# Kernel optimization log

Measured on AMD Instinct MI355X. Metric: run time of the kernel, lower is better.

## Reference

```python
import jax, jax.numpy as jnp
import numpy as np

S, B, I = 512, 32, 512
H, O = 512, 512
TOP_K = 5
TRUNC = 100
EPS = 1e-7
NEG = -1e9


def setup_inputs() -> dict:
    key = jax.random.key(0)
    ks = jax.random.split(key, 12)
    std = 1.0 / np.sqrt(H)
    return {
        "input": jax.random.normal(ks[0], (S, B, I), jnp.float32),
        "h0": jax.random.normal(ks[1], (1, B, H), jnp.float32),
        "c0": jax.random.normal(ks[2], (1, B, H), jnp.float32),
        "mem0": jax.random.normal(ks[3], (1, B, H), jnp.float32),
        # LSTMCell params (PyTorch layout: gates ordered i, f, g, o)
        "w_ih": jax.random.uniform(ks[4], (4 * H, I), jnp.float32, -std, std),
        "w_hh": jax.random.uniform(ks[5], (4 * H, H), jnp.float32, -std, std),
        "b_ih": jax.random.uniform(ks[6], (4 * H,), jnp.float32, -std, std),
        "b_hh": jax.random.uniform(ks[7], (4 * H,), jnp.float32, -std, std),
        # attention scorer, init N(0, 0.01)
        "w_t": jax.random.normal(ks[8], (2 * H, 1), jnp.float32) * 0.01,
        "fc_w": jax.random.uniform(ks[9], (O, 2 * H), jnp.float32, -1.0 / np.sqrt(2 * H), 1.0 / np.sqrt(2 * H)),
        "fc_b": jax.random.uniform(ks[10], (O,), jnp.float32, -1.0 / np.sqrt(2 * H), 1.0 / np.sqrt(2 * H)),
    }


def _sab_forward(input, h0, c0, mem0, w_ih, w_hh, b_ih, b_hh, w_t, fc_w, fc_b):
    seq_len, batch, _ = input.shape
    hid = w_hh.shape[1]
    m0 = mem0.shape[0]
    mmax = m0 + seq_len  # remem_every_k == 1: one append per step
    mem_buf = jnp.zeros((mmax, batch, hid), input.dtype).at[:m0].set(mem0)
    pos = jnp.arange(mmax)

    def step(carry, xs):
        h, c, mem = carry
        x, i = xs
        trunc = ((i + 1) % TRUNC) == 0
        h_in = jnp.where(trunc, jax.lax.stop_gradient(h), h)
        c_in = jnp.where(trunc, jax.lax.stop_gradient(c), c)
        # LSTM cell
        gates = x @ w_ih.T + b_ih + h_in @ w_hh.T + b_hh
        gi, gf, gg, go = jnp.split(gates, 4, axis=1)
        c_new = jax.nn.sigmoid(gf) * c_in + jax.nn.sigmoid(gi) * jnp.tanh(gg)
        h_new = jax.nn.sigmoid(go) * jnp.tanh(c_new)
        # attention over current (valid) memory
        cur = m0 + i  # valid memory entries before appending
        valid = (pos < cur)[:, None]  # (mmax, 1)
        feat = jnp.tanh(jnp.concatenate([jnp.broadcast_to(h_new[None], (mmax, batch, hid)), mem], axis=2))
        scores = jnp.einsum("mbf,fo->mb", feat, w_t)  # (mmax, batch)
        s_mask = jnp.where(valid, scores, NEG)
        kth = jax.lax.top_k(s_mask.T, TOP_K)[0][:, -1]  # (batch,)
        min_valid = jnp.min(jnp.where(valid, scores, jnp.inf), axis=0)
        delta = jnp.where(cur <= TOP_K, min_valid, kth) + EPS
        aw = jnp.clip(s_mask - delta[None, :], 0.0)  # invalid rows -> 0
        aw = aw / (jnp.sum(aw, axis=0, keepdims=True) + EPS)
        m_t = jnp.einsum("mb,mbh->bh", aw, mem)
        h_out = h_new + m_t
        mem = jax.lax.dynamic_update_slice(mem, h_out[None], (cur, 0, 0))
        return (h_out, c_new, mem), (h_out, m_t)

    (h_f, c_f, mem_f), (h_seq, m_seq) = jax.lax.scan(
        step, (h0[0], c0[0], mem_buf), (input, jnp.arange(seq_len)))
    out = jnp.concatenate([h_seq, m_seq], axis=2) @ fc_w.T + fc_b  # (S,B,O)
    return out, h_f[None], c_f[None], mem_f


def reference(input, h0, c0, mem0, w_ih, w_hh, b_ih, b_hh, w_t, fc_w, fc_b):
    return _sab_forward(input, h0, c0, mem0, w_ih, w_hh, b_ih, b_hh, w_t, fc_w, fc_b)
```

## Files before the change

kernel.cpp:

```cpp
#include <hip/hip_runtime.h>

#define SEQ   512
#define NB    32
#define NH    512
#define BH    16384
#define EPSF  1e-7f
#define NWG   64

#define HF_OFF  8388608
#define CF_OFF  8404992
#define MEM_OFF 8421376

#define X0_OFF   0ul
#define X1_OFF   16777216ul
#define WI0_OFF  33554432ul
#define WI1_OFF  35651584ul
#define HH_OFF   37748736ul
#define HMF_OFF  54558720ul
#define MSEQ_OFF 71368704ul
#define FCW_OFF  88145920ul
#define S2P_OFF  89194496ul
#define BAR_OFF  93396992ul
#define GX_OFF   93405184ul

typedef __attribute__((ext_vector_type(8))) short bf16x8;
typedef __attribute__((ext_vector_type(4))) float f32x4;
typedef __attribute__((ext_vector_type(4))) int   i32x4;

__device__ __forceinline__ unsigned short f2bf(float f){
  unsigned u = __float_as_uint(f);
  unsigned r = (u + 0x7fffu + ((u >> 16) & 1u)) >> 16;
  return (unsigned short)r;
}
__device__ __forceinline__ float bf2f(unsigned short h){
  return __uint_as_float(((unsigned)h) << 16);
}
__device__ __forceinline__ float sigmf(float x){ return 1.f/(1.f + __expf(-x)); }
__device__ __forceinline__ float tanhff(float x){
  x = fminf(20.f, fmaxf(-20.f, x));
  float e = __expf(-2.f*x);
  return (1.f - e)/(1.f + e);
}

__device__ __forceinline__ void store16_cc(void* p, i32x4 v){
  asm volatile("global_store_dwordx4 %0, %1, off sc0 sc1" :: "v"(p), "v"(v) : "memory");
}

__global__ void phase0(const float* __restrict__ x, const float* __restrict__ h0,
                       const float* __restrict__ mem0, const float* __restrict__ fcw,
                       const float* __restrict__ wih,
                       unsigned short* __restrict__ x0, unsigned short* __restrict__ x1,
                       unsigned short* __restrict__ wi0, unsigned short* __restrict__ wi1,
                       unsigned short* __restrict__ hh, unsigned short* __restrict__ hmf,
                       unsigned short* __restrict__ fcwb,
                       float* __restrict__ mem_row0, unsigned* __restrict__ bar){
  long i = (long)blockIdx.x * blockDim.x + threadIdx.x;
  if (i < (long)SEQ*BH){
    float v = x[i];
    unsigned short a = f2bf(v);
    x0[i]=a; x1[i]=f2bf(v - bf2f(a));
  }
  if (i < 2048*512){
    float v = wih[i];
    unsigned short a = f2bf(v);
    wi0[i]=a; wi1[i]=f2bf(v - bf2f(a));
  }
  if (i < 512*1024) fcwb[i] = f2bf(fcw[i]);
  if (i < BH){
    float h = h0[i];
    unsigned short a = f2bf(h);
    int b = (int)(i >> 9), col = (int)(i & 511);
    long d = (long)(col>>3)*256 + b*8 + (col&7);
    hh[d]=a; hmf[d]=f2bf(h - bf2f(a));
    mem_row0[i] = mem0[i];
  }
  if (i < 2048) bar[i] = 0u;
}

__launch_bounds__(256)
__global__ void xgemm(const unsigned short* __restrict__ x0, const unsigned short* __restrict__ x1,
                      const unsigned short* __restrict__ wi0, const unsigned short* __restrict__ wi1,
                      const float* __restrict__ bih, const float* __restrict__ bhh,
                      float* __restrict__ gx){
  const int tid = threadIdx.x;
  const int wave = tid >> 6, lane = tid & 63, quad = lane >> 4, ln = lane & 15;
  const int rowb = blockIdx.x*64 + wave*16;
  const int colb = blockIdx.y*64;
  const long aoff = (long)(rowb + ln)*512 + quad*8;
  f32x4 acc[4] = {{0,0,0,0},{0,0,0,0},{0,0,0,0},{0,0,0,0}};
  #pragma unroll 4
  for (int ki = 0; ki < 16; ++ki){
    bf16x8 a0 = *(const bf16x8*)(x0 + aoff + ki*32);
    bf16x8 a1 = *(const bf16x8*)(x1 + aoff + ki*32);
    #pragma unroll
    for (int n = 0; n < 4; ++n){
      long bo = (long)(colb + n*16 + ln)*512 + quad*8 + ki*32;
      bf16x8 b0 = *(const bf16x8*)(wi0 + bo);
      bf16x8 b1 = *(const bf16x8*)(wi1 + bo);
      acc[n] = __builtin_amdgcn_mfma_f32_16x16x32_bf16(a0, b0, acc[n], 0,0,0);
      acc[n] = __builtin_amdgcn_mfma_f32_16x16x32_bf16(a0, b1, acc[n], 0,0,0);
      acc[n] = __builtin_amdgcn_mfma_f32_16x16x32_bf16(a1, b0, acc[n], 0,0,0);
    }
  }
  #pragma unroll
  for (int n = 0; n < 4; ++n){
    int col = colb + n*16 + ln;
    float bias = bih[col] + bhh[col];
    #pragma unroll
    for (int rr = 0; rr < 4; ++rr){
      int row = rowb + quad*4 + rr;
      gx[(long)row*2048 + col] = acc[n][rr] + bias;
    }
  }
}

__launch_bounds__(256, 1)
__global__ void recurrent(unsigned short* __restrict__ hh,
                          unsigned short* __restrict__ hmf,
                          unsigned short* __restrict__ mseq,
                          float* __restrict__ s2p,
                          unsigned* __restrict__ bar,
                          float* __restrict__ dout,
                          const float* __restrict__ gx,
                          const float* __restrict__ whh,
                          const float* __restrict__ wt,
                          const float* __restrict__ c0){
  const int g    = blockIdx.x;
  const int tid  = threadIdx.x;
  const int wave = tid >> 6, lane = tid & 63, quad = lane >> 4, ln = lane & 15;
  const int mtile = wave & 1, ntile = wave >> 1;

  __shared__ float gates_lds[32*33];
  __shared__ float wt_lds[32*5];
  __shared__ int   idx_lds[32*5];
  __shared__ unsigned hm_lds[256];
  __shared__ float s2_lds[32];

  bf16x8 fW0[16], fW1[16];
  {
    int cl   = ntile*16 + ln;
    int gate = cl >> 3, jl = cl & 7;
    long grow = (long)(gate*NH + g*8 + jl);
    const float* wh = whh + grow*NH;
    #pragma unroll
    for (int ki = 0; ki < 16; ++ki){
      int k0 = ki*32 + quad*8;
      bf16x8 a, b;
      #pragma unroll
      for (int e = 0; e < 8; ++e){
        float vh = wh[k0+e];
        unsigned short w0 = f2bf(vh);
        a[e] = (short)w0; b[e] = (short)f2bf(vh - bf2f(w0));
      }
      fW0[ki]=a; fW1[ki]=b;
    }
  }

  const int b_  = tid >> 3, jl_ = tid & 7;
  const int jg_ = g*8 + jl_;
  const float wt2 = wt[NH + jg_];
  float creg = c0[b_*NH + jg_];
  float* memf = dout + MEM_OFF;

  {
    float v = tanhff(memf[b_*NH + jg_]) * wt2;
    v += __shfl_xor(v, 1); v += __shfl_xor(v, 2); v += __shfl_xor(v, 4);
    if (jl_ == 0)
      __hip_atomic_store((unsigned*)(s2p + g*32 + b_), __float_as_uint(v),
                         __ATOMIC_RELAXED, __HIP_MEMORY_SCOPE_AGENT);
  }

  const float* gxr0 = gx + (long)b_*2048 + jg_;
  float gxi = gxr0[0], gxf = gxr0[512], gxg = gxr0[1024], gxo = gxr0[1536];

  float tv0=-3e38f,tv1=-3e38f,tv2=-3e38f,tv3=-3e38f,tv4=-3e38f;
  int   ti0=0,ti1=0,ti2=0,ti3=0,ti4=0;

  unsigned epoch = 1u;
  __syncthreads();
  if (tid == 0)
    __hip_atomic_store(&bar[g*32], epoch, __ATOMIC_RELAXED, __HIP_MEMORY_SCOPE_AGENT);
  if (tid < 64){
    while (true){
      unsigned v = __hip_atomic_load(&bar[tid*32], __ATOMIC_RELAXED, __HIP_MEMORY_SCOPE_AGENT);
      if (__all((int)(v >= epoch))) break;
    }
  }
  __syncthreads();

  const int arow = mtile*16 + ln;

  #pragma unroll 1
  for (int t = 0; t < SEQ; ++t){
    if (tid < 32){
      const float* sp = s2p + (long)t*2048 + tid;
      float s0=0.f,s1=0.f,s2v=0.f,s3=0.f;
      #pragma unroll
      for (int q = 0; q < 64; q += 4){
        s0  += sp[(q  )*32];
        s1  += sp[(q+1)*32];
        s2v += sp[(q+2)*32];
        s3  += sp[(q+3)*32];
      }
      float s = (s0+s1) + (s2v+s3);
      if (t < 5){
        if      (t==0){tv0=s;ti0=0;}
        else if (t==1){tv1=s;ti1=1;}
        else if (t==2){tv2=s;ti2=2;}
        else if (t==3){tv3=s;ti3=3;}
        else          {tv4=s;ti4=4;}
      } else {
        float mn = fminf(fminf(fminf(tv0,tv1),fminf(tv2,tv3)),tv4);
        if (s > mn){
          if      (tv0==mn){tv0=s;ti0=t;}
          else if (tv1==mn){tv1=s;ti1=t;}
          else if (tv2==mn){tv2=s;ti2=t;}
          else if (tv3==mn){tv3=s;ti3=t;}
          else             {tv4=s;ti4=t;}
        }
      }
      int cnt = (t+1 < 5) ? (t+1) : 5;
      float mn = tv0;
      if (cnt>1) mn = fminf(mn, tv1);
      if (cnt>2) mn = fminf(mn, tv2);
      if (cnt>3) mn = fminf(mn, tv3);
      if (cnt>4) mn = fminf(mn, tv4);
      float thr = mn + EPSF;
      float w0 =            fmaxf(tv0-thr,0.f);
      float w1 = (cnt>1) ? fmaxf(tv1-thr,0.f) : 0.f;
      float w2 = (cnt>2) ? fmaxf(tv2-thr,0.f) : 0.f;
      float w3 = (cnt>3) ? fmaxf(tv3-thr,0.f) : 0.f;
      float w4 = (cnt>4) ? fmaxf(tv4-thr,0.f) : 0.f;
      float inv = 1.f/((w0+w1+w2+w3+w4) + EPSF);
      wt_lds[tid*5+0]=w0*inv; idx_lds[tid*5+0]=ti0;
      wt_lds[tid*5+1]=w1*inv; idx_lds[tid*5+1]=ti1;
      wt_lds[tid*5+2]=w2*inv; idx_lds[tid*5+2]=ti2;
      wt_lds[tid*5+3]=w3*inv; idx_lds[tid*5+3]=ti3;
      wt_lds[tid*5+4]=w4*inv; idx_lds[tid*5+4]=ti4;
    }

    const unsigned short* p0 = hh  + (long)t*BH + quad*256 + arow*8;
    const unsigned short* p1 = hmf + (long)t*BH + quad*256 + arow*8;
    f32x4 acc0 = {0.f,0.f,0.f,0.f}, acc1 = {0.f,0.f,0.f,0.f};
    #pragma unroll
    for (int ki = 0; ki < 16; ++ki){
      bf16x8 aH = *(const bf16x8*)(p0 + ki*1024);
      bf16x8 aM = *(const bf16x8*)(p1 + ki*1024);
      acc0 = __builtin_amdgcn_mfma_f32_16x16x32_bf16(aH, fW0[ki], acc0, 0,0,0);
      acc1 = __builtin_amdgcn_mfma_f32_16x16x32_bf16(aH, fW1[ki], acc1, 0,0,0);
      if (ki & 1) acc1 = __builtin_amdgcn_mfma_f32_16x16x32_bf16(aM, fW0[ki], acc1, 0,0,0);
      else        acc0 = __builtin_amdgcn_mfma_f32_16x16x32_bf16(aM, fW0[ki], acc0, 0,0,0);
    }
    #pragma unroll
    for (int r = 0; r < 4; ++r){
      int brow = mtile*16 + quad*4 + r;
      gates_lds[brow*33 + ntile*16 + ln] = acc0[r] + acc1[r];
    }
    __syncthreads();

    float g0 = gates_lds[b_*33 + jl_     ] + gxi;
    float g1 = gates_lds[b_*33 +  8 + jl_] + gxf;
    float g2 = gates_lds[b_*33 + 16 + jl_] + gxg;
    float g3 = gates_lds[b_*33 + 24 + jl_] + gxo;
    float ig = sigmf(g0), fg = sigmf(g1), gg = tanhff(g2), og = sigmf(g3);
    creg = fg*creg + ig*gg;
    float hn = og * tanhff(creg);
    float mt = 0.f;
    #pragma unroll
    for (int l = 0; l < 5; ++l){
      float w = wt_lds[b_*5 + l];
      int  id = idx_lds[b_*5 + l];
      mt += w * memf[(long)id*BH + b_*NH + jg_];
    }
    float ho = hn + mt;
    long eoff = (long)b_*NH + jg_;
    memf[(long)(t+1)*BH + eoff] = ho;
    unsigned short h0s = f2bf(ho);
    unsigned short h1s = f2bf(ho - bf2f(h0s));
    hm_lds[b_*8 + jl_] = (unsigned)h0s | (((unsigned)h1s) << 16);
    mseq[(long)t*BH + eoff] = f2bf(mt);
    if (t == SEQ-1) dout[HF_OFF + eoff] = ho;

    {
      float v = tanhff(ho) * wt2;
      v += __shfl_xor(v, 1); v += __shfl_xor(v, 2); v += __shfl_xor(v, 4);
      if (jl_ == 0) s2_lds[b_] = v;
    }

    {
      int tn = (t+1 < SEQ) ? t+1 : t;
      const float* gxr = gx + ((long)tn*32 + b_)*2048 + jg_;
      gxi = gxr[0]; gxf = gxr[512]; gxg = gxr[1024]; gxo = gxr[1536];
    }

    __syncthreads();
    if (tid < 32){
      int b = tid;
      unsigned q0 = hm_lds[b*8+0], q1 = hm_lds[b*8+1], q2 = hm_lds[b*8+2], q3 = hm_lds[b*8+3];
      unsigned q4 = hm_lds[b*8+4], q5 = hm_lds[b*8+5], q6 = hm_lds[b*8+6], q7 = hm_lds[b*8+7];
      i32x4 hi, mi;
      hi[0] = (int)((q0 & 0xffffu) | (q1 << 16));
      hi[1] = (int)((q2 & 0xffffu) | (q3 << 16));
      hi[2] = (int)((q4 & 0xffffu) | (q5 << 16));
      hi[3] = (int)((q6 & 0xffffu) | (q7 << 16));
      mi[0] = (int)((q0 >> 16) | (q1 & 0xffff0000u));
      mi[1] = (int)((q2 >> 16) | (q3 & 0xffff0000u));
      mi[2] = (int)((q4 >> 16) | (q5 & 0xffff0000u));
      mi[3] = (int)((q6 >> 16) | (q7 & 0xffff0000u));
      long d = (long)(t+1)*BH + g*256 + b*8;
      store16_cc(hh  + d, hi);
      store16_cc(hmf + d, mi);
    } else if (tid < 40){
      int q = tid - 32;
      f32x4 sv = *(const f32x4*)&s2_lds[q*4];
      store16_cc(s2p + (long)(t+1)*2048 + g*32 + q*4, __builtin_bit_cast(i32x4, sv));
    }
    __syncthreads();
    ++epoch;
    if (tid == 0)
      __hip_atomic_store(&bar[g*32], epoch, __ATOMIC_RELAXED, __HIP_MEMORY_SCOPE_AGENT);
    if (tid < 64){
      while (true){
        unsigned v = __hip_atomic_load(&bar[tid*32], __ATOMIC_RELAXED, __HIP_MEMORY_SCOPE_AGENT);
        if (__all((int)(v >= epoch))) break;
      }
    }
    __syncthreads();
  }
  dout[CF_OFF + (long)b_*NH + jg_] = creg;
}

__launch_bounds__(256)
__global__ void outgemm(const unsigned short* __restrict__ hh,
                        const unsigned short* __restrict__ mseq,
                        const unsigned short* __restrict__ fcwb,
                        const float* __restrict__ fcb,
                        float* __restrict__ out){
  const int tid = threadIdx.x;
  const int wave = tid >> 6, lane = tid & 63, quad = lane >> 4, ln = lane & 15;
  const int wgM = blockIdx.x;
  const int wgN = blockIdx.y;
  const int r = wgM*64 + wave*16 + ln;
  const int s = r >> 5, b = r & 31;
  const unsigned short* pa_h = hh   + (long)(s+1)*BH + quad*256 + b*8;
  const unsigned short* pa_m = mseq + (long)s*BH     + (long)b*NH + quad*8;
  const unsigned short* pb   = fcwb + (long)(wgN*64 + ln)*1024 + quad*8;
  f32x4 accs[4] = {{0,0,0,0},{0,0,0,0},{0,0,0,0},{0,0,0,0}};
  #pragma unroll 4
  for (int ki = 0; ki < 16; ++ki){
    bf16x8 a = *(const bf16x8*)(pa_h + ki*1024);
    #pragma unroll
    for (int n = 0; n < 4; ++n){
      bf16x8 bb = *(const bf16x8*)(pb + (long)n*16*1024 + ki*32);
      accs[n] = __builtin_amdgcn_mfma_f32_16x16x32_bf16(a, bb, accs[n], 0,0,0);
    }
  }
  #pragma unroll 4
  for (int ki = 0; ki < 16; ++ki){
    bf16x8 a = *(const bf16x8*)(pa_m + ki*32);
    #pragma unroll
    for (int n = 0; n < 4; ++n){
      bf16x8 bb = *(const bf16x8*)(pb + 512 + (long)n*16*1024 + ki*32);
      accs[n] = __builtin_amdgcn_mfma_f32_16x16x32_bf16(a, bb, accs[n], 0,0,0);
    }
  }
  #pragma unroll
  for (int n = 0; n < 4; ++n){
    int o = wgN*64 + n*16 + ln;
    float bias = fcb[o];
    #pragma unroll
    for (int rr = 0; rr < 4; ++rr){
      int row = wgM*64 + wave*16 + quad*4 + rr;
      out[(long)row*512 + o] = accs[n][rr] + bias;
    }
  }
}

extern "C" void kernel_launch(void* const* d_in, const int* in_sizes, int n_in,
                              void* d_out, int out_size, void* d_ws, size_t ws_size,
                              hipStream_t stream){
  (void)in_sizes; (void)n_in; (void)out_size; (void)ws_size;
  const float* x    = (const float*)d_in[0];
  const float* h0   = (const float*)d_in[1];
  const float* c0   = (const float*)d_in[2];
  const float* mem0 = (const float*)d_in[3];
  const float* wih  = (const float*)d_in[4];
  const float* whh  = (const float*)d_in[5];
  const float* bih  = (const float*)d_in[6];
  const float* bhh  = (const float*)d_in[7];
  const float* wt   = (const float*)d_in[8];
  const float* fcw  = (const float*)d_in[9];
  const float* fcb  = (const float*)d_in[10];
  float* out = (float*)d_out;
  char* ws = (char*)d_ws;

  unsigned short* x0   = (unsigned short*)(ws + X0_OFF);
  unsigned short* x1   = (unsigned short*)(ws + X1_OFF);
  unsigned short* wi0  = (unsigned short*)(ws + WI0_OFF);
  unsigned short* wi1  = (unsigned short*)(ws + WI1_OFF);
  unsigned short* hh   = (unsigned short*)(ws + HH_OFF);
  unsigned short* hmf  = (unsigned short*)(ws + HMF_OFF);
  unsigned short* mseq = (unsigned short*)(ws + MSEQ_OFF);
  unsigned short* fcwb = (unsigned short*)(ws + FCW_OFF);
  float*          s2p  = (float*)(ws + S2P_OFF);
  unsigned*       bar  = (unsigned*)(ws + BAR_OFF);
  float*          gx   = (float*)(ws + GX_OFF);

  phase0<<<32768, 256, 0, stream>>>(x, h0, mem0, fcw, wih,
                                    x0, x1, wi0, wi1,
                                    hh, hmf, fcwb, out + MEM_OFF, bar);
  xgemm<<<dim3(256, 32), 256, 0, stream>>>(x0, x1, wi0, wi1, bih, bhh, gx);
  recurrent<<<NWG, 256, 0, stream>>>(hh, hmf, mseq, s2p, bar, out,
                                     gx, whh, wt, c0);
  outgemm<<<dim3(256, 8), 256, 0, stream>>>(hh, mseq, fcwb, fcb, out);
}
```

Measured before the change: 3.895 ms.

## Pin persistent recurrent workgroups to a single XCC and stage activations via LDS

The recurrent kernel now launches 4096 workgroups. Each reads its XCC id and takes a ticket, and the first XCC to collect 64 tickets becomes the only active one, so all cross-workgroup barrier traffic stays inside one XCC's L2. Because of that, the cache-bypassing sc0/sc1 stores are replaced with plain stores. Per step, three waves copy the h/mem bf16 activation tiles into LDS with global_load_lds, and the gathered memory reads for the attention sum are issued early. This adds launch overhead and relies on the plain stores being coherent within one XCC, which risks stale reads if that assumption fails.

```diff
diff --git a/kernel.cpp b/kernel.cpp
--- a/kernel.cpp
+++ b/kernel.cpp
@@ -40,10 +40,6 @@
   x = fminf(20.f, fmaxf(-20.f, x));
   float e = __expf(-2.f*x);
   return (1.f - e)/(1.f + e);
-}
-
-__device__ __forceinline__ void store16_cc(void* p, i32x4 v){
-  asm volatile("global_store_dwordx4 %0, %1, off sc0 sc1" :: "v"(p), "v"(v) : "memory");
 }
 
 __global__ void phase0(const float* __restrict__ x, const float* __restrict__ h0,
@@ -114,7 +110,7 @@
   }
 }
 
-__launch_bounds__(256, 1)
+__launch_bounds__(256, 2)
 __global__ void recurrent(unsigned short* __restrict__ hh,
                           unsigned short* __restrict__ hmf,
                           unsigned short* __restrict__ mseq,
@@ -125,16 +121,44 @@
                           const float* __restrict__ whh,
                           const float* __restrict__ wt,
                           const float* __restrict__ c0){
-  const int g    = blockIdx.x;
   const int tid  = threadIdx.x;
-  const int wave = tid >> 6, lane = tid & 63, quad = lane >> 4, ln = lane & 15;
-  const int mtile = wave & 1, ntile = wave >> 1;
-
+
+  __shared__ unsigned short aHi[16384];
+  __shared__ unsigned short aMd[16384];
   __shared__ float gates_lds[32*33];
   __shared__ float wt_lds[32*5];
   __shared__ int   idx_lds[32*5];
   __shared__ unsigned hm_lds[256];
   __shared__ float s2_lds[32];
+  __shared__ int   s_g;
+
+  if (tid == 0){
+    unsigned xcc;
+    asm volatile("s_getreg_b32 %0, hwreg(HW_REG_XCC_ID)" : "=s"(xcc));
+    xcc &= 7u;
+    unsigned tk = __hip_atomic_fetch_add(&bar[16 + xcc], 1u,
+                    __ATOMIC_RELAXED, __HIP_MEMORY_SCOPE_AGENT);
+    int gg = -1;
+    if (tk < NWG){
+      if (tk == NWG - 1){
+        unsigned exp = 0u;
+        __hip_atomic_compare_exchange_strong(&bar[8], &exp, xcc + 1u,
+            __ATOMIC_RELAXED, __ATOMIC_RELAXED, __HIP_MEMORY_SCOPE_AGENT);
+      }
+      unsigned wv;
+      do {
+        wv = __hip_atomic_load(&bar[8], __ATOMIC_RELAXED, __HIP_MEMORY_SCOPE_AGENT);
+      } while (wv == 0u);
+      if (wv == xcc + 1u) gg = (int)tk;
+    }
+    s_g = gg;
+  }
+  __syncthreads();
+  const int g = s_g;
+  if (g < 0) return;
+
+  const int wave = tid >> 6, lane = tid & 63, quad = lane >> 4, ln = lane & 15;
+  const int mtile = wave & 1, ntile = wave >> 1;
 
   bf16x8 fW0[16], fW1[16];
   {
@@ -165,9 +189,7 @@
   {
     float v = tanhff(memf[b_*NH + jg_]) * wt2;
     v += __shfl_xor(v, 1); v += __shfl_xor(v, 2); v += __shfl_xor(v, 4);
-    if (jl_ == 0)
-      __hip_atomic_store((unsigned*)(s2p + g*32 + b_), __float_as_uint(v),
-                         __ATOMIC_RELAXED, __HIP_MEMORY_SCOPE_AGENT);
+    if (jl_ == 0) s2p[g*32 + b_] = v;
   }
 
   const float* gxr0 = gx + (long)b_*2048 + jg_;
@@ -188,10 +210,28 @@
   }
   __syncthreads();
 
-  const int arow = mtile*16 + ln;
+  const int abase = quad*256 + (mtile*16 + ln)*8;
 
   #pragma unroll 1
   for (int t = 0; t < SEQ; ++t){
+    if (wave){
+      const unsigned short* srcH = hh  + (long)t*BH;
+      const unsigned short* srcM = hmf + (long)t*BH;
+      const int cnt = (wave == 3) ? 22 : 21;
+      const int cb  = 21*(wave - 1);
+      #pragma unroll 1
+      for (int i = 0; i < cnt; ++i){
+        const int c = cb + i;
+        const unsigned short* s;
+        unsigned short* d;
+        if (c < 32){ s = srcH + c*512 + lane*8;      d = aHi + c*512; }
+        else       { s = srcM + (c-32)*512 + lane*8; d = aMd + (c-32)*512; }
+        __builtin_amdgcn_global_load_lds(
+            (const __attribute__((address_space(1))) void*)s,
+            (__attribute__((address_space(3))) void*)d, 16, 0, 0);
+      }
+    }
+
     if (tid < 32){
       const float* sp = s2p + (long)t*2048 + tid;
       float s0=0.f,s1=0.f,s2v=0.f,s3=0.f;
@@ -239,13 +279,25 @@
       wt_lds[tid*5+4]=w4*inv; idx_lds[tid*5+4]=ti4;
     }
 
-    const unsigned short* p0 = hh  + (long)t*BH + quad*256 + arow*8;
-    const unsigned short* p1 = hmf + (long)t*BH + quad*256 + arow*8;
+    __syncthreads();
+
+    const long eoff = (long)b_*NH + jg_;
+    const float w0a = wt_lds[b_*5+0]; const int i0a = idx_lds[b_*5+0];
+    const float w1a = wt_lds[b_*5+1]; const int i1a = idx_lds[b_*5+1];
+    const float w2a = wt_lds[b_*5+2]; const int i2a = idx_lds[b_*5+2];
+    const float w3a = wt_lds[b_*5+3]; const int i3a = idx_lds[b_*5+3];
+    const float w4a = wt_lds[b_*5+4]; const int i4a = idx_lds[b_*5+4];
+    const float v0a = memf[(long)i0a*BH + eoff];
+    const float v1a = memf[(long)i1a*BH + eoff];
+    const float v2a = memf[(long)i2a*BH + eoff];
+    const float v3a = memf[(long)i3a*BH + eoff];
+    const float v4a = memf[(long)i4a*BH + eoff];
+
     f32x4 acc0 = {0.f,0.f,0.f,0.f}, acc1 = {0.f,0.f,0.f,0.f};
     #pragma unroll
     for (int ki = 0; ki < 16; ++ki){
-      bf16x8 aH = *(const bf16x8*)(p0 + ki*1024);
-      bf16x8 aM = *(const bf16x8*)(p1 + ki*1024);
+      bf16x8 aH = *(const bf16x8*)(aHi + abase + ki*1024);
+      bf16x8 aM = *(const bf16x8*)(aMd + abase + ki*1024);
       acc0 = __builtin_amdgcn_mfma_f32_16x16x32_bf16(aH, fW0[ki], acc0, 0,0,0);
       acc1 = __builtin_amdgcn_mfma_f32_16x16x32_bf16(aH, fW1[ki], acc1, 0,0,0);
       if (ki & 1) acc1 = __builtin_amdgcn_mfma_f32_16x16x32_bf16(aM, fW0[ki], acc1, 0,0,0);
@@ -266,14 +318,8 @@
     creg = fg*creg + ig*gg;
     float hn = og * tanhff(creg);
     float mt = 0.f;
-    #pragma unroll
-    for (int l = 0; l < 5; ++l){
-      float w = wt_lds[b_*5 + l];
-      int  id = idx_lds[b_*5 + l];
-      mt += w * memf[(long)id*BH + b_*NH + jg_];
-    }
+    mt += w0a*v0a; mt += w1a*v1a; mt += w2a*v2a; mt += w3a*v3a; mt += w4a*v4a;
     float ho = hn + mt;
-    long eoff = (long)b_*NH + jg_;
     memf[(long)(t+1)*BH + eoff] = ho;
     unsigned short h0s = f2bf(ho);
     unsigned short h1s = f2bf(ho - bf2f(h0s));
@@ -308,12 +354,11 @@
       mi[2] = (int)((q4 >> 16) | (q5 & 0xffff0000u));
       mi[3] = (int)((q6 >> 16) | (q7 & 0xffff0000u));
       long d = (long)(t+1)*BH + g*256 + b*8;
-      store16_cc(hh  + d, hi);
-      store16_cc(hmf + d, mi);
+      *(i32x4*)(hh  + d) = hi;
+      *(i32x4*)(hmf + d) = mi;
     } else if (tid < 40){
       int q = tid - 32;
-      f32x4 sv = *(const f32x4*)&s2_lds[q*4];
-      store16_cc(s2p + (long)(t+1)*2048 + g*32 + q*4, __builtin_bit_cast(i32x4, sv));
+      *(f32x4*)(s2p + (long)(t+1)*2048 + g*32 + q*4) = *(const f32x4*)&s2_lds[q*4];
     }
     __syncthreads();
     ++epoch;
@@ -410,7 +455,7 @@
                                     x0, x1, wi0, wi1,
                                     hh, hmf, fcwb, out + MEM_OFF, bar);
   xgemm<<<dim3(256, 32), 256, 0, stream>>>(x0, x1, wi0, wi1, bih, bhh, gx);
-  recurrent<<<NWG, 256, 0, stream>>>(hh, hmf, mseq, s2p, bar, out,
-                                     gx, whh, wt, c0);
+  recurrent<<<4096, 256, 0, stream>>>(hh, hmf, mseq, s2p, bar, out,
+                                      gx, whh, wt, c0);
   outgemm<<<dim3(256, 8), 256, 0, stream>>>(hh, mseq, fcwb, fcb, out);
 }
```

New measurement: 13.53 ms. 247% more time.

## Keep top-k memory values in registers and overlap score loads with MFMA

Applied to the files above, without the earlier changes.

Each thread now keeps the five selected memory values in registers and swaps in the previous output when the top-k set replaces a slot. This removes the per-step global gathers from the memory buffer. The partial-score loads are issued as vector loads before the gate MFMA and staged through LDS, so their latency hides behind the matrix work. The publish stores and barrier signal are folded into the first wave with an explicit vmcnt wait, which drops one block-wide __syncthreads per step. In exchange it uses more LDS and adds register-held state.

```diff
diff --git a/kernel.cpp b/kernel.cpp
--- a/kernel.cpp
+++ b/kernel.cpp
@@ -131,8 +131,9 @@
   const int mtile = wave & 1, ntile = wave >> 1;
 
   __shared__ float gates_lds[32*33];
+  __shared__ float s2v[64*33];
   __shared__ float wt_lds[32*5];
-  __shared__ int   idx_lds[32*5];
+  __shared__ int   repl_lds[32];
   __shared__ unsigned hm_lds[256];
   __shared__ float s2_lds[32];
 
@@ -162,8 +163,12 @@
   float creg = c0[b_*NH + jg_];
   float* memf = dout + MEM_OFF;
 
+  float m0v = memf[b_*NH + jg_];
+  float va0 = 0.f, va1 = 0.f, va2 = 0.f, va3 = 0.f, va4 = 0.f;
+  float hoprev = m0v;
+
   {
-    float v = tanhff(memf[b_*NH + jg_]) * wt2;
+    float v = tanhff(m0v) * wt2;
     v += __shfl_xor(v, 1); v += __shfl_xor(v, 2); v += __shfl_xor(v, 4);
     if (jl_ == 0)
       __hip_atomic_store((unsigned*)(s2p + g*32 + b_), __float_as_uint(v),
@@ -174,7 +179,6 @@
   float gxi = gxr0[0], gxf = gxr0[512], gxg = gxr0[1024], gxo = gxr0[1536];
 
   float tv0=-3e38f,tv1=-3e38f,tv2=-3e38f,tv3=-3e38f,tv4=-3e38f;
-  int   ti0=0,ti1=0,ti2=0,ti3=0,ti4=0;
 
   unsigned epoch = 1u;
   __syncthreads();
@@ -192,31 +196,66 @@
 
   #pragma unroll 1
   for (int t = 0; t < SEQ; ++t){
+    f32x4 sv0, sv1, sv2, sv3, sv4, sv5, sv6, sv7;
+    if (tid < 64){
+      const float* sp = s2p + (long)t*2048 + tid*32;
+      sv0 = *(const f32x4*)(sp +  0); sv1 = *(const f32x4*)(sp +  4);
+      sv2 = *(const f32x4*)(sp +  8); sv3 = *(const f32x4*)(sp + 12);
+      sv4 = *(const f32x4*)(sp + 16); sv5 = *(const f32x4*)(sp + 20);
+      sv6 = *(const f32x4*)(sp + 24); sv7 = *(const f32x4*)(sp + 28);
+    }
+
+    const unsigned short* p0 = hh  + (long)t*BH + quad*256 + arow*8;
+    const unsigned short* p1 = hmf + (long)t*BH + quad*256 + arow*8;
+    f32x4 acc0 = {0.f,0.f,0.f,0.f}, acc1 = {0.f,0.f,0.f,0.f};
+    #pragma unroll
+    for (int ki = 0; ki < 16; ++ki){
+      bf16x8 aH = *(const bf16x8*)(p0 + ki*1024);
+      bf16x8 aM = *(const bf16x8*)(p1 + ki*1024);
+      acc0 = __builtin_amdgcn_mfma_f32_16x16x32_bf16(aH, fW0[ki], acc0, 0,0,0);
+      acc1 = __builtin_amdgcn_mfma_f32_16x16x32_bf16(aH, fW1[ki], acc1, 0,0,0);
+      if (ki & 1) acc1 = __builtin_amdgcn_mfma_f32_16x16x32_bf16(aM, fW0[ki], acc1, 0,0,0);
+      else        acc0 = __builtin_amdgcn_mfma_f32_16x16x32_bf16(aM, fW0[ki], acc0, 0,0,0);
+    }
+    #pragma unroll
+    for (int r = 0; r < 4; ++r){
+      int brow = mtile*16 + quad*4 + r;
+      gates_lds[brow*33 + ntile*16 + ln] = acc0[r] + acc1[r];
+    }
+
+    if (tid < 64){
+      float* sr = &s2v[tid*33];
+      *(f32x4*)(sr +  0) = sv0; *(f32x4*)(sr +  4) = sv1;
+      *(f32x4*)(sr +  8) = sv2; *(f32x4*)(sr + 12) = sv3;
+      *(f32x4*)(sr + 16) = sv4; *(f32x4*)(sr + 20) = sv5;
+      *(f32x4*)(sr + 24) = sv6; *(f32x4*)(sr + 28) = sv7;
+    }
     if (tid < 32){
-      const float* sp = s2p + (long)t*2048 + tid;
-      float s0=0.f,s1=0.f,s2v=0.f,s3=0.f;
+      float s0=0.f,s1=0.f,s2s=0.f,s3=0.f;
       #pragma unroll
       for (int q = 0; q < 64; q += 4){
-        s0  += sp[(q  )*32];
-        s1  += sp[(q+1)*32];
-        s2v += sp[(q+2)*32];
-        s3  += sp[(q+3)*32];
+        s0  += s2v[(q  )*33 + tid];
+        s1  += s2v[(q+1)*33 + tid];
+        s2s += s2v[(q+2)*33 + tid];
+        s3  += s2v[(q+3)*33 + tid];
       }
-      float s = (s0+s1) + (s2v+s3);
+      float s = (s0+s1) + (s2s+s3);
+      int repl = -1;
       if (t < 5){
-        if      (t==0){tv0=s;ti0=0;}
-        else if (t==1){tv1=s;ti1=1;}
-        else if (t==2){tv2=s;ti2=2;}
-        else if (t==3){tv3=s;ti3=3;}
-        else          {tv4=s;ti4=4;}
+        repl = t;
+        if      (t==0) tv0=s;
+        else if (t==1) tv1=s;
+        else if (t==2) tv2=s;
+        else if (t==3) tv3=s;
+        else           tv4=s;
       } else {
         float mn = fminf(fminf(fminf(tv0,tv1),fminf(tv2,tv3)),tv4);
         if (s > mn){
-          if      (tv0==mn){tv0=s;ti0=t;}
-          else if (tv1==mn){tv1=s;ti1=t;}
-          else if (tv2==mn){tv2=s;ti2=t;}
-          else if (tv3==mn){tv3=s;ti3=t;}
-          else             {tv4=s;ti4=t;}
+          if      (tv0==mn){tv0=s;repl=0;}
+          else if (tv1==mn){tv1=s;repl=1;}
+          else if (tv2==mn){tv2=s;repl=2;}
+          else if (tv3==mn){tv3=s;repl=3;}
+          else             {tv4=s;repl=4;}
         }
       }
       int cnt = (t+1 < 5) ? (t+1) : 5;
@@ -232,29 +271,12 @@
       float w3 = (cnt>3) ? fmaxf(tv3-thr,0.f) : 0.f;
       float w4 = (cnt>4) ? fmaxf(tv4-thr,0.f) : 0.f;
       float inv = 1.f/((w0+w1+w2+w3+w4) + EPSF);
-      wt_lds[tid*5+0]=w0*inv; idx_lds[tid*5+0]=ti0;
-      wt_lds[tid*5+1]=w1*inv; idx_lds[tid*5+1]=ti1;
-      wt_lds[tid*5+2]=w2*inv; idx_lds[tid*5+2]=ti2;
-      wt_lds[tid*5+3]=w3*inv; idx_lds[tid*5+3]=ti3;
-      wt_lds[tid*5+4]=w4*inv; idx_lds[tid*5+4]=ti4;
-    }
-
-    const unsigned short* p0 = hh  + (long)t*BH + quad*256 + arow*8;
-    const unsigned short* p1 = hmf + (long)t*BH + quad*256 + arow*8;
-    f32x4 acc0 = {0.f,0.f,0.f,0.f}, acc1 = {0.f,0.f,0.f,0.f};
-    #pragma unroll
-    for (int ki = 0; ki < 16; ++ki){
-      bf16x8 aH = *(const bf16x8*)(p0 + ki*1024);
-      bf16x8 aM = *(const bf16x8*)(p1 + ki*1024);
-      acc0 = __builtin_amdgcn_mfma_f32_16x16x32_bf16(aH, fW0[ki], acc0, 0,0,0);
-      acc1 = __builtin_amdgcn_mfma_f32_16x16x32_bf16(aH, fW1[ki], acc1, 0,0,0);
-      if (ki & 1) acc1 = __builtin_amdgcn_mfma_f32_16x16x32_bf16(aM, fW0[ki], acc1, 0,0,0);
-      else        acc0 = __builtin_amdgcn_mfma_f32_16x16x32_bf16(aM, fW0[ki], acc0, 0,0,0);
-    }
-    #pragma unroll
-    for (int r = 0; r < 4; ++r){
-      int brow = mtile*16 + quad*4 + r;
-      gates_lds[brow*33 + ntile*16 + ln] = acc0[r] + acc1[r];
+      wt_lds[tid*5+0]=w0*inv;
+      wt_lds[tid*5+1]=w1*inv;
+      wt_lds[tid*5+2]=w2*inv;
+      wt_lds[tid*5+3]=w3*inv;
+      wt_lds[tid*5+4]=w4*inv;
+      repl_lds[tid]=repl;
     }
     __syncthreads();
 
@@ -265,13 +287,15 @@
     float ig = sigmf(g0), fg = sigmf(g1), gg = tanhff(g2), og = sigmf(g3);
     creg = fg*creg + ig*gg;
     float hn = og * tanhff(creg);
-    float mt = 0.f;
-    #pragma unroll
-    for (int l = 0; l < 5; ++l){
-      float w = wt_lds[b_*5 + l];
-      int  id = idx_lds[b_*5 + l];
-      mt += w * memf[(long)id*BH + b_*NH + jg_];
-    }
+
+    int rp = repl_lds[b_];
+    va0 = (rp==0) ? hoprev : va0;
+    va1 = (rp==1) ? hoprev : va1;
+    va2 = (rp==2) ? hoprev : va2;
+    va3 = (rp==3) ? hoprev : va3;
+    va4 = (rp==4) ? hoprev : va4;
+    float mt = wt_lds[b_*5+0]*va0 + wt_lds[b_*5+1]*va1 + wt_lds[b_*5+2]*va2
+             + wt_lds[b_*5+3]*va3 + wt_lds[b_*5+4]*va4;
     float ho = hn + mt;
     long eoff = (long)b_*NH + jg_;
     memf[(long)(t+1)*BH + eoff] = ho;
@@ -280,6 +304,7 @@
     hm_lds[b_*8 + jl_] = (unsigned)h0s | (((unsigned)h1s) << 16);
     mseq[(long)t*BH + eoff] = f2bf(mt);
     if (t == SEQ-1) dout[HF_OFF + eoff] = ho;
+    hoprev = ho;
 
     {
       float v = tanhff(ho) * wt2;
@@ -294,32 +319,32 @@
     }
 
     __syncthreads();
-    if (tid < 32){
-      int b = tid;
-      unsigned q0 = hm_lds[b*8+0], q1 = hm_lds[b*8+1], q2 = hm_lds[b*8+2], q3 = hm_lds[b*8+3];
-      unsigned q4 = hm_lds[b*8+4], q5 = hm_lds[b*8+5], q6 = hm_lds[b*8+6], q7 = hm_lds[b*8+7];
-      i32x4 hi, mi;
-      hi[0] = (int)((q0 & 0xffffu) | (q1 << 16));
-      hi[1] = (int)((q2 & 0xffffu) | (q3 << 16));
-      hi[2] = (int)((q4 & 0xffffu) | (q5 << 16));
-      hi[3] = (int)((q6 & 0xffffu) | (q7 << 16));
-      mi[0] = (int)((q0 >> 16) | (q1 & 0xffff0000u));
-      mi[1] = (int)((q2 >> 16) | (q3 & 0xffff0000u));
-      mi[2] = (int)((q4 >> 16) | (q5 & 0xffff0000u));
-      mi[3] = (int)((q6 >> 16) | (q7 & 0xffff0000u));
-      long d = (long)(t+1)*BH + g*256 + b*8;
-      store16_cc(hh  + d, hi);
-      store16_cc(hmf + d, mi);
-    } else if (tid < 40){
-      int q = tid - 32;
-      f32x4 sv = *(const f32x4*)&s2_lds[q*4];
-      store16_cc(s2p + (long)(t+1)*2048 + g*32 + q*4, __builtin_bit_cast(i32x4, sv));
-    }
-    __syncthreads();
     ++epoch;
-    if (tid == 0)
-      __hip_atomic_store(&bar[g*32], epoch, __ATOMIC_RELAXED, __HIP_MEMORY_SCOPE_AGENT);
     if (tid < 64){
+      if (tid < 32){
+        int b = tid;
+        unsigned q0 = hm_lds[b*8+0], q1 = hm_lds[b*8+1], q2 = hm_lds[b*8+2], q3 = hm_lds[b*8+3];
+        unsigned q4 = hm_lds[b*8+4], q5 = hm_lds[b*8+5], q6 = hm_lds[b*8+6], q7 = hm_lds[b*8+7];
+        i32x4 hi, mi;
+        hi[0] = (int)((q0 & 0xffffu) | (q1 << 16));
+        hi[1] = (int)((q2 & 0xffffu) | (q3 << 16));
+        hi[2] = (int)((q4 & 0xffffu) | (q5 << 16));
+        hi[3] = (int)((q6 & 0xffffu) | (q7 << 16));
+        mi[0] = (int)((q0 >> 16) | (q1 & 0xffff0000u));
+        mi[1] = (int)((q2 >> 16) | (q3 & 0xffff0000u));
+        mi[2] = (int)((q4 >> 16) | (q5 & 0xffff0000u));
+        mi[3] = (int)((q6 >> 16) | (q7 & 0xffff0000u));
+        long d = (long)(t+1)*BH + g*256 + b*8;
+        store16_cc(hh  + d, hi);
+        store16_cc(hmf + d, mi);
+      } else if (tid < 40){
+        int q = tid - 32;
+        f32x4 svp = *(const f32x4*)&s2_lds[q*4];
+        store16_cc(s2p + (long)(t+1)*2048 + g*32 + q*4, __builtin_bit_cast(i32x4, svp));
+      }
+      asm volatile("s_waitcnt vmcnt(0)" ::: "memory");
+      if (tid == 0)
+        __hip_atomic_store(&bar[g*32], epoch, __ATOMIC_RELAXED, __HIP_MEMORY_SCOPE_AGENT);
       while (true){
         unsigned v = __hip_atomic_load(&bar[tid*32], __ATOMIC_RELAXED, __HIP_MEMORY_SCOPE_AGENT);
         if (__all((int)(v >= epoch))) break;
```

After: 4.561 ms. +17.1%, slower.
